# Performance work log

Hardware: AMD Instinct MI355X
Metric: run time of the kernel (lower is better)

## Reference

```python
import jax, jax.numpy as jnp
import numpy as np

B, IN, H = 16384, 1024, 1024


def setup_inputs() -> dict:
    key = jax.random.key(0)
    ks = jax.random.split(key, 16)
    stdv = 1.0 / np.sqrt(H)
    u = lambda k, shape: jax.random.uniform(k, shape, jnp.float32, -stdv, stdv)
    return {
        "input": jax.random.normal(ks[0], (B, IN), jnp.float32),
        "prev_h": jax.random.normal(ks[1], (B, H), jnp.float32),
        "prev_c": jax.random.normal(ks[2], (B, H), jnp.float32),
        "weight_xi": u(ks[3], (IN, H)), "weight_hi": u(ks[4], (H, H)),
        "weight_xf": u(ks[5], (IN, H)), "weight_hf": u(ks[6], (H, H)),
        "weight_xu": u(ks[7], (IN, H)), "weight_hu": u(ks[8], (H, H)),
        "weight_xo": u(ks[9], (IN, H)), "weight_ho": u(ks[10], (H, H)),
        "bias_i": u(ks[11], (H,)), "bias_f": u(ks[12], (H,)),
        "bias_o": u(ks[13], (H,)), "bias_u": u(ks[14], (H,)),
    }


def reference(input, prev_h, prev_c,
              weight_xi, weight_hi, weight_xf, weight_hf,
              weight_xu, weight_hu, weight_xo, weight_ho,
              bias_i, bias_f, bias_o, bias_u):
    i = jax.nn.sigmoid(input @ weight_xi + prev_h @ weight_hi + bias_i)
    f = jax.nn.sigmoid(input @ weight_xf + prev_h @ weight_hf + bias_f)
    o = jax.nn.sigmoid(input @ weight_xo + prev_h @ weight_ho + bias_o)
    u = jnp.tanh(input @ weight_xu + prev_h @ weight_hu + bias_u)
    c = f * prev_c + i * u
    h = o * jnp.tanh(c)
    return (h, c)
```

## Files before the change

kernel.cpp:

```cpp
#include <hip/hip_runtime.h>
#include <hip/hip_bf16.h>
#include <stdint.h>
#include <type_traits>


typedef short bf16x8 __attribute__((ext_vector_type(8)));
typedef unsigned short u16x8 __attribute__((ext_vector_type(8)));
typedef float f32x16 __attribute__((ext_vector_type(16)));

__device__ __forceinline__ unsigned short f2bf(float f) {
    union { float f; uint32_t u; } v; v.f = f;
    uint32_t r = v.u + 0x7FFFu + ((v.u >> 16) & 1u);
    return (unsigned short)(r >> 16);
}

__device__ __forceinline__ float fsig(float x) { return 1.0f / (1.0f + __expf(-x)); }
__device__ __forceinline__ float ftanh(float x) { return 2.0f * fsig(2.0f * x) - 1.0f; }

__global__ __launch_bounds__(256) void pack_a_kernel(const float* __restrict__ input,
                                                     const float* __restrict__ prev_h,
                                                     unsigned short* __restrict__ Apk2) {
    int u = blockIdx.x * 256 + threadIdx.x;
    int l = u & 63, q = (u >> 6) & 1, rg = (u >> 7) & 7, t = (u >> 10) & 63, rt = u >> 16;
    int row = rt * 256 + rg * 32 + (l & 31);
    int k0 = t * 32 + (q * 2 + (l >> 5)) * 8;
    const float* src = (k0 < 1024) ? (input + (size_t)row * 1024 + k0)
                                   : (prev_h + (size_t)row * 1024 + (k0 - 1024));
    float4 lo = *(const float4*)src;
    float4 hi = *(const float4*)(src + 4);
    u16x8 o;
    o[0] = f2bf(lo.x); o[1] = f2bf(lo.y); o[2] = f2bf(lo.z); o[3] = f2bf(lo.w);
    o[4] = f2bf(hi.x); o[5] = f2bf(hi.y); o[6] = f2bf(hi.z); o[7] = f2bf(hi.w);
    *(u16x8*)(Apk2 + (size_t)u * 8) = o;
}

__global__ __launch_bounds__(256) void pack_b_kernel(
        const float* __restrict__ wxi, const float* __restrict__ wxf,
        const float* __restrict__ wxo, const float* __restrict__ wxu,
        const float* __restrict__ whi, const float* __restrict__ whf,
        const float* __restrict__ who, const float* __restrict__ whu,
        unsigned short* __restrict__ Bpk2) {
    int u = blockIdx.x * 256 + threadIdx.x;
    int l = u & 63, q = (u >> 6) & 1, ch = (u >> 7) & 1, g = (u >> 8) & 3,
        t = (u >> 10) & 63, ct = u >> 16;
    const float* wx = (g == 0) ? wxi : (g == 1) ? wxf : (g == 2) ? wxo : wxu;
    const float* wh = (g == 0) ? whi : (g == 1) ? whf : (g == 2) ? who : whu;
    int j = ct * 64 + ch * 32 + (l & 31);
    int k0 = t * 32 + (q * 2 + (l >> 5)) * 8;
    const float* src = (k0 < 1024) ? (wx + (size_t)k0 * 1024 + j)
                                   : (wh + (size_t)(k0 - 1024) * 1024 + j);
    u16x8 o;
#pragma unroll
    for (int e = 0; e < 8; ++e) o[e] = f2bf(src[(size_t)e * 1024]);
    *(u16x8*)(Bpk2 + (size_t)u * 8) = o;
}


#define GLL(gp, lp) __builtin_amdgcn_global_load_lds( \
        (__attribute__((address_space(1))) void*)(gp), \
        (__attribute__((address_space(3))) void*)(lp), 16, 0, 0)

#define BAR() do { asm volatile("" ::: "memory"); __builtin_amdgcn_s_barrier(); \
                   asm volatile("" ::: "memory"); } while (0)

__global__ __launch_bounds__(512, 2) void lstm_gemm_kernel(
        const unsigned short* __restrict__ Apk2,
        const unsigned short* __restrict__ Bpk2,
        const float* __restrict__ prev_c,
        const float* __restrict__ bi, const float* __restrict__ bf_,
        const float* __restrict__ bo, const float* __restrict__ bu,
        float* __restrict__ out_h, float* __restrict__ out_c) {
    __shared__ __align__(16) unsigned char smem[131072];
    const int tid = threadIdx.x;
    const int w = tid >> 6, l = tid & 63;
    const int l31 = l & 31, l5 = l >> 5;
    const int wr = w >> 1, wc = w & 1;

    const int bid = blockIdx.x;
    const int sw = ((bid & 7) << 7) + (bid >> 3);
    const int tileRow = sw & 63, tileCol = sw >> 6;
    const int rowBase = tileRow * 256;
    const int jBase = tileCol * 64;

    int aoff[2][2], boff[4][2];
#pragma unroll
    for (int m = 0; m < 2; ++m)
#pragma unroll
        for (int ks = 0; ks < 2; ++ks)
            aoff[m][ks] = (wr * 2 + m) * 2048 + (ks * 2 + l5) * 512 + l31 * 16;
#pragma unroll
    for (int g = 0; g < 4; ++g)
#pragma unroll
        for (int ks = 0; ks < 2; ++ks)
            boff[g][ks] = 16384 + g * 4096 + wc * 2048 + (ks * 2 + l5) * 512 + l31 * 16;

    const unsigned short* aSrc = Apk2 + (size_t)tileRow * 64 * 8192 + w * 1024 + l * 8;
    const unsigned short* bSrc = Bpk2 + (size_t)tileCol * 64 * 8192
                               + (w >> 1) * 2048 + (w & 1) * 1024 + l * 8;
    const int aD = w * 2048;
    const int bD = 16384 + (w >> 1) * 4096 + (w & 1) * 2048;

#define STAGE4(T) do { const int _bb = ((T) & 3) * 32768; \
        const size_t _o = (size_t)(T) * 8192; \
        GLL(aSrc + _o,       smem + _bb + aD); \
        GLL(aSrc + _o + 512, smem + _bb + aD + 1024); \
        GLL(bSrc + _o,       smem + _bb + bD); \
        GLL(bSrc + _o + 512, smem + _bb + bD + 1024); } while (0)

    f32x16 acc[2][4];
#pragma unroll
    for (int m = 0; m < 2; ++m)
#pragma unroll
        for (int g = 0; g < 4; ++g)
#pragma unroll
            for (int q = 0; q < 16; ++q) acc[m][g][q] = 0.f;

    STAGE4(0); STAGE4(1);
    asm volatile("s_waitcnt vmcnt(4)" ::: "memory");
    BAR();

    auto slice = [&](int t, auto vnc, auto stgc) {
        constexpr int VN = decltype(vnc)::value;
        constexpr bool STG = decltype(stgc)::value;
        const int bt = (t & 3) * 32768;
        if constexpr (STG) STAGE4(t + 2);
        bf16x8 av[2][2], bv[4][2];
#pragma unroll
        for (int m = 0; m < 2; ++m)
#pragma unroll
            for (int ks = 0; ks < 2; ++ks)
                av[m][ks] = *(const bf16x8*)(smem + bt + aoff[m][ks]);
#pragma unroll
        for (int g = 0; g < 4; ++g)
#pragma unroll
            for (int ks = 0; ks < 2; ++ks)
                bv[g][ks] = *(const bf16x8*)(smem + bt + boff[g][ks]);
#pragma unroll
        for (int ks = 0; ks < 2; ++ks)
#pragma unroll
            for (int m = 0; m < 2; ++m)
#pragma unroll
                for (int g = 0; g < 4; ++g)
                    acc[m][g] = __builtin_amdgcn_mfma_f32_32x32x16_bf16(
                        av[m][ks], bv[g][ks], acc[m][g], 0, 0, 0);
        if constexpr (VN == 4)      asm volatile("s_waitcnt vmcnt(4)" ::: "memory");
        else if constexpr (VN == 0) asm volatile("s_waitcnt vmcnt(0)" ::: "memory");
        if constexpr (VN >= 0) BAR();
    };

    using c4 = std::integral_constant<int, 4>;
    using c0 = std::integral_constant<int, 0>;
    using cm = std::integral_constant<int, -1>;
    using bT = std::integral_constant<bool, true>;
    using bF = std::integral_constant<bool, false>;

#pragma unroll 1
    for (int t = 0; t < 62; ++t) slice(t, c4{}, bT{});
    slice(62, c0{}, bF{});
    slice(63, cm{}, bF{});

    const int colIdx = jBase + wc * 32 + l31;
    const float vbi = bi[colIdx], vbf = bf_[colIdx], vbo = bo[colIdx], vbu = bu[colIdx];
    const int rowB = rowBase + wr * 64 + 4 * l5;
#pragma unroll
    for (int m = 0; m < 2; ++m) {
#pragma unroll
        for (int q = 0; q < 16; ++q) {
            const int row = rowB + m * 32 + (q & 3) + 8 * (q >> 2);
            const size_t idx = (size_t)row * 1024 + colIdx;
            float zi = acc[m][0][q] + vbi;
            float zf = acc[m][1][q] + vbf;
            float zo = acc[m][2][q] + vbo;
            float zu = acc[m][3][q] + vbu;
            float iv = fsig(zi), fv = fsig(zf), ov = fsig(zo), uv = ftanh(zu);
            float cv = fv * prev_c[idx] + iv * uv;
            out_c[idx] = cv;
            out_h[idx] = ov * ftanh(cv);
        }
    }
#undef STAGE4
}

extern "C" void kernel_launch(void* const* d_in, const int* in_sizes, int n_in,
                              void* d_out, int out_size, void* d_ws, size_t ws_size,
                              hipStream_t stream) {
    const float* input  = (const float*)d_in[0];
    const float* prev_h = (const float*)d_in[1];
    const float* prev_c = (const float*)d_in[2];
    const float* wxi = (const float*)d_in[3];
    const float* whi = (const float*)d_in[4];
    const float* wxf = (const float*)d_in[5];
    const float* whf = (const float*)d_in[6];
    const float* wxu = (const float*)d_in[7];
    const float* whu = (const float*)d_in[8];
    const float* wxo = (const float*)d_in[9];
    const float* who = (const float*)d_in[10];
    const float* bi  = (const float*)d_in[11];
    const float* bf_ = (const float*)d_in[12];
    const float* bo  = (const float*)d_in[13];
    const float* bu  = (const float*)d_in[14];

    unsigned short* Apk2 = (unsigned short*)d_ws;
    unsigned short* Bpk2 = (unsigned short*)((char*)d_ws + (size_t)67108864);

    float* out_h = (float*)d_out;
    float* out_c = out_h + (size_t)16384 * 1024;

    pack_a_kernel<<<dim3(16384), dim3(256), 0, stream>>>(input, prev_h, Apk2);
    pack_b_kernel<<<dim3(4096), dim3(256), 0, stream>>>(wxi, wxf, wxo, wxu,
                                                        whi, whf, who, whu, Bpk2);
    lstm_gemm_kernel<<<dim3(1024), dim3(512), 0, stream>>>(Apk2, Bpk2, prev_c,
                                                           bi, bf_, bo, bu, out_h, out_c);
}
```

Before: 349.9 us.

## Deepen LDS prefetch to three stages and double-buffer MFMA fragments in registers

Global-to-LDS staging now runs three K-slices ahead instead of two, using the existing four LDS buffers. The shared-memory reads of operand fragments for slice t+1 are issued during the MFMAs of slice t, into alternating register sets. sched_group_barrier hints interleave those LDS reads with the MFMA instructions. The aim is to hide LDS and global latency behind the matrix math, at the cost of more VGPRs for the doubled fragment buffers, which could lower occupancy or cause spills.

```diff
diff --git a/kernel.cpp b/kernel.cpp
--- a/kernel.cpp
+++ b/kernel.cpp
@@ -115,26 +115,35 @@
 #pragma unroll
             for (int q = 0; q < 16; ++q) acc[m][g][q] = 0.f;
 
-    STAGE4(0); STAGE4(1);
+    bf16x8 aE[4], bE[8], aO[4], bO[8];
+
+    auto ldfr = [&](int t, bf16x8 (&da)[4], bf16x8 (&db)[8]) {
+        const int bt = (t & 3) * 32768;
+#pragma unroll
+        for (int m = 0; m < 2; ++m)
+#pragma unroll
+            for (int ks = 0; ks < 2; ++ks)
+                da[m * 2 + ks] = *(const bf16x8*)(smem + bt + aoff[m][ks]);
+#pragma unroll
+        for (int g = 0; g < 4; ++g)
+#pragma unroll
+            for (int ks = 0; ks < 2; ++ks)
+                db[g * 2 + ks] = *(const bf16x8*)(smem + bt + boff[g][ks]);
+    };
+
+    STAGE4(0); STAGE4(1); STAGE4(2);
     asm volatile("s_waitcnt vmcnt(4)" ::: "memory");
     BAR();
-
-    auto slice = [&](int t, auto vnc, auto stgc) {
+    ldfr(0, aE, bE);
+
+    auto slice = [&](int t, auto vnc, auto stgc, auto nxtc,
+                     bf16x8 (&ca)[4], bf16x8 (&cb)[8],
+                     bf16x8 (&na)[4], bf16x8 (&nb)[8]) {
         constexpr int VN = decltype(vnc)::value;
         constexpr bool STG = decltype(stgc)::value;
-        const int bt = (t & 3) * 32768;
-        if constexpr (STG) STAGE4(t + 2);
-        bf16x8 av[2][2], bv[4][2];
-#pragma unroll
-        for (int m = 0; m < 2; ++m)
-#pragma unroll
-            for (int ks = 0; ks < 2; ++ks)
-                av[m][ks] = *(const bf16x8*)(smem + bt + aoff[m][ks]);
-#pragma unroll
-        for (int g = 0; g < 4; ++g)
-#pragma unroll
-            for (int ks = 0; ks < 2; ++ks)
-                bv[g][ks] = *(const bf16x8*)(smem + bt + boff[g][ks]);
+        constexpr bool NXT = decltype(nxtc)::value;
+        if constexpr (STG) STAGE4(t + 3);
+        if constexpr (NXT) ldfr(t + 1, na, nb);
 #pragma unroll
         for (int ks = 0; ks < 2; ++ks)
 #pragma unroll
@@ -142,7 +151,11 @@
 #pragma unroll
                 for (int g = 0; g < 4; ++g)
                     acc[m][g] = __builtin_amdgcn_mfma_f32_32x32x16_bf16(
-                        av[m][ks], bv[g][ks], acc[m][g], 0, 0, 0);
+                        ca[m * 2 + ks], cb[g * 2 + ks], acc[m][g], 0, 0, 0);
+        if constexpr (NXT) {
+            __builtin_amdgcn_sched_group_barrier(0x100, 12, 0);
+            __builtin_amdgcn_sched_group_barrier(0x8,   16, 0);
+        }
         if constexpr (VN == 4)      asm volatile("s_waitcnt vmcnt(4)" ::: "memory");
         else if constexpr (VN == 0) asm volatile("s_waitcnt vmcnt(0)" ::: "memory");
         if constexpr (VN >= 0) BAR();
@@ -155,9 +168,14 @@
     using bF = std::integral_constant<bool, false>;
 
 #pragma unroll 1
-    for (int t = 0; t < 62; ++t) slice(t, c4{}, bT{});
-    slice(62, c0{}, bF{});
-    slice(63, cm{}, bF{});
+    for (int t = 0; t < 60; t += 2) {
+        slice(t,     c4{}, bT{}, bT{}, aE, bE, aO, bO);
+        slice(t + 1, c4{}, bT{}, bT{}, aO, bO, aE, bE);
+    }
+    slice(60, c4{}, bT{}, bT{}, aE, bE, aO, bO);
+    slice(61, c0{}, bF{}, bT{}, aO, bO, aE, bE);
+    slice(62, cm{}, bF{}, bT{}, aE, bE, aO, bO);
+    slice(63, cm{}, bF{}, bF{}, aO, bO, aE, bE);
 
     const int colIdx = jBase + wc * 32 + l31;
     const float vbi = bi[colIdx], vbf = bf_[colIdx], vbo = bo[colIdx], vbu = bu[colIdx];
```

New measurement: 372.9 us. +6.6%, slower.

## Load A fragments directly into registers, stage only B through LDS

Applied to the files above, without the earlier changes.

The A operand is now read straight from global memory into double-buffered registers (one slice ahead) instead of being staged through LDS. LDS then holds only the B tiles, which halves its footprint to 64 KB, and the wait counts are adjusted for the mixed load stream. The aim is to cut LDS traffic and capacity pressure, which could allow more resident blocks. In exchange it raises register pressure, and because each wave pair loads its A rows separately, some A data is fetched from global memory twice.

```diff
diff --git a/kernel.cpp b/kernel.cpp
--- a/kernel.cpp
+++ b/kernel.cpp
@@ -70,7 +70,7 @@
         const float* __restrict__ bi, const float* __restrict__ bf_,
         const float* __restrict__ bo, const float* __restrict__ bu,
         float* __restrict__ out_h, float* __restrict__ out_c) {
-    __shared__ __align__(16) unsigned char smem[131072];
+    __shared__ __align__(16) unsigned char smem[65536];
     const int tid = threadIdx.x;
     const int w = tid >> 6, l = tid & 63;
     const int l31 = l & 31, l5 = l >> 5;
@@ -82,28 +82,20 @@
     const int rowBase = tileRow * 256;
     const int jBase = tileCol * 64;
 
-    int aoff[2][2], boff[4][2];
-#pragma unroll
-    for (int m = 0; m < 2; ++m)
+    int boff[4][2];
+#pragma unroll
+    for (int g = 0; g < 4; ++g)
 #pragma unroll
         for (int ks = 0; ks < 2; ++ks)
-            aoff[m][ks] = (wr * 2 + m) * 2048 + (ks * 2 + l5) * 512 + l31 * 16;
-#pragma unroll
-    for (int g = 0; g < 4; ++g)
-#pragma unroll
-        for (int ks = 0; ks < 2; ++ks)
-            boff[g][ks] = 16384 + g * 4096 + wc * 2048 + (ks * 2 + l5) * 512 + l31 * 16;
-
-    const unsigned short* aSrc = Apk2 + (size_t)tileRow * 64 * 8192 + w * 1024 + l * 8;
-    const unsigned short* bSrc = Bpk2 + (size_t)tileCol * 64 * 8192
-                               + (w >> 1) * 2048 + (w & 1) * 1024 + l * 8;
-    const int aD = w * 2048;
-    const int bD = 16384 + (w >> 1) * 4096 + (w & 1) * 2048;
-
-#define STAGE4(T) do { const int _bb = ((T) & 3) * 32768; \
+            boff[g][ks] = g * 4096 + wc * 2048 + (ks * 2 + l5) * 512 + l31 * 16;
+
+    const unsigned short* aSrcF = Apk2 + (size_t)tileRow * 524288 + (wr * 2) * 1024 + l * 8;
+
+    const unsigned short* bSrc = Bpk2 + (size_t)tileCol * 524288 + w * 1024 + l * 8;
+    const int bD = w * 2048;
+
+#define STAGE_B(T) do { const int _bb = ((T) & 3) * 16384; \
         const size_t _o = (size_t)(T) * 8192; \
-        GLL(aSrc + _o,       smem + _bb + aD); \
-        GLL(aSrc + _o + 512, smem + _bb + aD + 1024); \
         GLL(bSrc + _o,       smem + _bb + bD); \
         GLL(bSrc + _o + 512, smem + _bb + bD + 1024); } while (0)
 
@@ -115,21 +107,31 @@
 #pragma unroll
             for (int q = 0; q < 16; ++q) acc[m][g][q] = 0.f;
 
-    STAGE4(0); STAGE4(1);
-    asm volatile("s_waitcnt vmcnt(4)" ::: "memory");
+    bf16x8 aE[4], aO[4];
+
+    auto ldA = [&](int t, bf16x8 (&da)[4]) {
+        const unsigned short* ap = aSrcF + (size_t)t * 8192;
+#pragma unroll
+        for (int m = 0; m < 2; ++m)
+#pragma unroll
+            for (int ks = 0; ks < 2; ++ks)
+                da[m * 2 + ks] = *(const bf16x8*)(ap + m * 1024 + ks * 512);
+    };
+
+    ldA(0, aE);
+    STAGE_B(0); STAGE_B(1);
+    asm volatile("s_waitcnt vmcnt(2)" ::: "memory");
     BAR();
 
-    auto slice = [&](int t, auto vnc, auto stgc) {
+    auto slice = [&](int t, auto vnc, auto stgc, auto ldac,
+                     bf16x8 (&aCur)[4], bf16x8 (&aNxt)[4]) {
         constexpr int VN = decltype(vnc)::value;
         constexpr bool STG = decltype(stgc)::value;
-        const int bt = (t & 3) * 32768;
-        if constexpr (STG) STAGE4(t + 2);
-        bf16x8 av[2][2], bv[4][2];
-#pragma unroll
-        for (int m = 0; m < 2; ++m)
-#pragma unroll
-            for (int ks = 0; ks < 2; ++ks)
-                av[m][ks] = *(const bf16x8*)(smem + bt + aoff[m][ks]);
+        constexpr bool LDA = decltype(ldac)::value;
+        const int bt = (t & 3) * 16384;
+        if constexpr (LDA) ldA(t + 1, aNxt);
+        if constexpr (STG) STAGE_B(t + 2);
+        bf16x8 bv[4][2];
 #pragma unroll
         for (int g = 0; g < 4; ++g)
 #pragma unroll
@@ -142,22 +144,25 @@
 #pragma unroll
                 for (int g = 0; g < 4; ++g)
                     acc[m][g] = __builtin_amdgcn_mfma_f32_32x32x16_bf16(
-                        av[m][ks], bv[g][ks], acc[m][g], 0, 0, 0);
-        if constexpr (VN == 4)      asm volatile("s_waitcnt vmcnt(4)" ::: "memory");
-        else if constexpr (VN == 0) asm volatile("s_waitcnt vmcnt(0)" ::: "memory");
+                        aCur[m * 2 + ks], bv[g][ks], acc[m][g], 0, 0, 0);
+        if constexpr (VN == 6)      asm volatile("s_waitcnt vmcnt(6)" ::: "memory");
+        else if constexpr (VN == 4) asm volatile("s_waitcnt vmcnt(4)" ::: "memory");
         if constexpr (VN >= 0) BAR();
     };
 
+    using c6 = std::integral_constant<int, 6>;
     using c4 = std::integral_constant<int, 4>;
-    using c0 = std::integral_constant<int, 0>;
     using cm = std::integral_constant<int, -1>;
     using bT = std::integral_constant<bool, true>;
     using bF = std::integral_constant<bool, false>;
 
 #pragma unroll 1
-    for (int t = 0; t < 62; ++t) slice(t, c4{}, bT{});
-    slice(62, c0{}, bF{});
-    slice(63, cm{}, bF{});
+    for (int t = 0; t < 62; t += 2) {
+        slice(t,     c6{}, bT{}, bT{}, aE, aO);
+        slice(t + 1, c6{}, bT{}, bT{}, aO, aE);
+    }
+    slice(62, c4{}, bF{}, bT{}, aE, aO);
+    slice(63, cm{}, bF{}, bF{}, aO, aE);
 
     const int colIdx = jBase + wc * 32 + l31;
     const float vbi = bi[colIdx], vbf = bf_[colIdx], vbo = bo[colIdx], vbu = bu[colIdx];
@@ -178,7 +183,7 @@
             out_h[idx] = ov * ftanh(cv);
         }
     }
-#undef STAGE4
+#undef STAGE_B
 }
 
 extern "C" void kernel_launch(void* const* d_in, const int* in_sizes, int n_in,
```

After: 372.1 us. 6.4% more time.

## Switch GEMM main loop to double-buffered 64-wide K tiles with interleaved staging

Applied to the files above, without the earlier changes.

Restructures the fused LSTM GEMM main loop from a 4-deep ring of 32-wide K slices (one barrier per slice) to a 2-buffer scheme with 64-wide K tiles of 64KB each. Global-to-LDS loads for the next tile are spread between the four MFMA sub-steps of the current tile, so there is one barrier per 64 K instead of per 32. The intent is to halve barrier and wait overhead and interleave loads with compute. The cost is a shallower prefetch distance with a full vmcnt(0) wait each tile, which may expose memory latency. The LDS offset math changes to match a new packed layout, and correctness depends on that layout agreeing with the unseen pack kernels.

```diff
diff --git a/kernel.cpp b/kernel.cpp
--- a/kernel.cpp
+++ b/kernel.cpp
@@ -82,30 +82,29 @@
     const int rowBase = tileRow * 256;
     const int jBase = tileCol * 64;
 
-    int aoff[2][2], boff[4][2];
+    int aoff[2][4], boff[4][4];
 #pragma unroll
     for (int m = 0; m < 2; ++m)
 #pragma unroll
-        for (int ks = 0; ks < 2; ++ks)
-            aoff[m][ks] = (wr * 2 + m) * 2048 + (ks * 2 + l5) * 512 + l31 * 16;
+        for (int ks = 0; ks < 4; ++ks)
+            aoff[m][ks] = (ks >> 1) * 16384 + ((wr * 2 + m) * 2 + (ks & 1)) * 1024 + l * 16;
 #pragma unroll
     for (int g = 0; g < 4; ++g)
 #pragma unroll
-        for (int ks = 0; ks < 2; ++ks)
-            boff[g][ks] = 16384 + g * 4096 + wc * 2048 + (ks * 2 + l5) * 512 + l31 * 16;
-
-    const unsigned short* aSrc = Apk2 + (size_t)tileRow * 64 * 8192 + w * 1024 + l * 8;
-    const unsigned short* bSrc = Bpk2 + (size_t)tileCol * 64 * 8192
-                               + (w >> 1) * 2048 + (w & 1) * 1024 + l * 8;
-    const int aD = w * 2048;
-    const int bD = 16384 + (w >> 1) * 4096 + (w & 1) * 2048;
-
-#define STAGE4(T) do { const int _bb = ((T) & 3) * 32768; \
-        const size_t _o = (size_t)(T) * 8192; \
-        GLL(aSrc + _o,       smem + _bb + aD); \
-        GLL(aSrc + _o + 512, smem + _bb + aD + 1024); \
-        GLL(bSrc + _o,       smem + _bb + bD); \
-        GLL(bSrc + _o + 512, smem + _bb + bD + 1024); } while (0)
+        for (int ks = 0; ks < 4; ++ks)
+            boff[g][ks] = 32768 + (ks >> 1) * 16384 + (g * 4 + wc * 2 + (ks & 1)) * 1024 + l * 16;
+
+    const unsigned short* aSrcW = Apk2 + (size_t)tileRow * 524288
+                                + (size_t)(w >> 2) * 8192 + ((w & 3) * 4) * 512 + l * 8;
+    const unsigned short* bSrcW = Bpk2 + (size_t)tileCol * 524288
+                                + (size_t)(w >> 2) * 8192 + ((w & 3) * 4) * 512 + l * 8;
+    const int aDstW = w * 4096;
+    const int bDstW = 32768 + w * 4096;
+
+#define STAGE_A1(KT, J) GLL(aSrcW + (size_t)(KT) * 16384 + (J) * 512, \
+                            smem + ((((KT) & 1)) * 65536) + aDstW + (J) * 1024)
+#define STAGE_B1(KT, J) GLL(bSrcW + (size_t)(KT) * 16384 + (J) * 512, \
+                            smem + ((((KT) & 1)) * 65536) + bDstW + (J) * 1024)
 
     f32x16 acc[2][4];
 #pragma unroll
@@ -115,49 +114,67 @@
 #pragma unroll
             for (int q = 0; q < 16; ++q) acc[m][g][q] = 0.f;
 
-    STAGE4(0); STAGE4(1);
-    asm volatile("s_waitcnt vmcnt(4)" ::: "memory");
+    STAGE_A1(0, 0); STAGE_A1(0, 1); STAGE_A1(0, 2); STAGE_A1(0, 3);
+    STAGE_B1(0, 0); STAGE_B1(0, 1); STAGE_B1(0, 2); STAGE_B1(0, 3);
+    asm volatile("s_waitcnt vmcnt(0)" ::: "memory");
     BAR();
 
-    auto slice = [&](int t, auto vnc, auto stgc) {
-        constexpr int VN = decltype(vnc)::value;
-        constexpr bool STG = decltype(stgc)::value;
-        const int bt = (t & 3) * 32768;
-        if constexpr (STG) STAGE4(t + 2);
-        bf16x8 av[2][2], bv[4][2];
-#pragma unroll
-        for (int m = 0; m < 2; ++m)
-#pragma unroll
-            for (int ks = 0; ks < 2; ++ks)
-                av[m][ks] = *(const bf16x8*)(smem + bt + aoff[m][ks]);
-#pragma unroll
-        for (int g = 0; g < 4; ++g)
-#pragma unroll
-            for (int ks = 0; ks < 2; ++ks)
-                bv[g][ks] = *(const bf16x8*)(smem + bt + boff[g][ks]);
-#pragma unroll
-        for (int ks = 0; ks < 2; ++ks)
-#pragma unroll
-            for (int m = 0; m < 2; ++m)
-#pragma unroll
-                for (int g = 0; g < 4; ++g)
-                    acc[m][g] = __builtin_amdgcn_mfma_f32_32x32x16_bf16(
-                        av[m][ks], bv[g][ks], acc[m][g], 0, 0, 0);
-        if constexpr (VN == 4)      asm volatile("s_waitcnt vmcnt(4)" ::: "memory");
-        else if constexpr (VN == 0) asm volatile("s_waitcnt vmcnt(0)" ::: "memory");
-        if constexpr (VN >= 0) BAR();
+    auto ktile = [&](int kt, auto modeC) {
+        constexpr int MODE = decltype(modeC)::value;
+        const int bufb = (kt & 1) * 65536;
+        bf16x8 av[2], bv[4];
+#pragma unroll
+        for (int m = 0; m < 2; ++m) av[m] = *(const bf16x8*)(smem + bufb + aoff[m][0]);
+#pragma unroll
+        for (int g = 0; g < 4; ++g) bv[g] = *(const bf16x8*)(smem + bufb + boff[g][0]);
+        if constexpr (MODE == 0) { STAGE_A1(kt + 1, 0); STAGE_A1(kt + 1, 1); }
+#pragma unroll
+        for (int m = 0; m < 2; ++m)
+#pragma unroll
+            for (int g = 0; g < 4; ++g)
+                acc[m][g] = __builtin_amdgcn_mfma_f32_32x32x16_bf16(av[m], bv[g], acc[m][g], 0, 0, 0);
+#pragma unroll
+        for (int m = 0; m < 2; ++m) av[m] = *(const bf16x8*)(smem + bufb + aoff[m][1]);
+#pragma unroll
+        for (int g = 0; g < 4; ++g) bv[g] = *(const bf16x8*)(smem + bufb + boff[g][1]);
+        if constexpr (MODE == 0) { STAGE_A1(kt + 1, 2); STAGE_A1(kt + 1, 3);
+                                   STAGE_B1(kt + 1, 0); STAGE_B1(kt + 1, 1); }
+#pragma unroll
+        for (int m = 0; m < 2; ++m)
+#pragma unroll
+            for (int g = 0; g < 4; ++g)
+                acc[m][g] = __builtin_amdgcn_mfma_f32_32x32x16_bf16(av[m], bv[g], acc[m][g], 0, 0, 0);
+#pragma unroll
+        for (int m = 0; m < 2; ++m) av[m] = *(const bf16x8*)(smem + bufb + aoff[m][2]);
+#pragma unroll
+        for (int g = 0; g < 4; ++g) bv[g] = *(const bf16x8*)(smem + bufb + boff[g][2]);
+        if constexpr (MODE == 0) { STAGE_B1(kt + 1, 2); STAGE_B1(kt + 1, 3); }
+#pragma unroll
+        for (int m = 0; m < 2; ++m)
+#pragma unroll
+            for (int g = 0; g < 4; ++g)
+                acc[m][g] = __builtin_amdgcn_mfma_f32_32x32x16_bf16(av[m], bv[g], acc[m][g], 0, 0, 0);
+#pragma unroll
+        for (int m = 0; m < 2; ++m) av[m] = *(const bf16x8*)(smem + bufb + aoff[m][3]);
+#pragma unroll
+        for (int g = 0; g < 4; ++g) bv[g] = *(const bf16x8*)(smem + bufb + boff[g][3]);
+        if constexpr (MODE == 0) {
+            asm volatile("s_waitcnt vmcnt(0)" ::: "memory");
+            BAR();
+        }
+#pragma unroll
+        for (int m = 0; m < 2; ++m)
+#pragma unroll
+            for (int g = 0; g < 4; ++g)
+                acc[m][g] = __builtin_amdgcn_mfma_f32_32x32x16_bf16(av[m], bv[g], acc[m][g], 0, 0, 0);
     };
 
-    using c4 = std::integral_constant<int, 4>;
-    using c0 = std::integral_constant<int, 0>;
-    using cm = std::integral_constant<int, -1>;
-    using bT = std::integral_constant<bool, true>;
-    using bF = std::integral_constant<bool, false>;
+    using m0 = std::integral_constant<int, 0>;
+    using m1 = std::integral_constant<int, 1>;
 
 #pragma unroll 1
-    for (int t = 0; t < 62; ++t) slice(t, c4{}, bT{});
-    slice(62, c0{}, bF{});
-    slice(63, cm{}, bF{});
+    for (int kt = 0; kt < 31; ++kt) ktile(kt, m0{});
+    ktile(31, m1{});
 
     const int colIdx = jBase + wc * 32 + l31;
     const float vbi = bi[colIdx], vbf = bf_[colIdx], vbo = bo[colIdx], vbu = bu[colIdx];
@@ -178,7 +195,8 @@
             out_h[idx] = ov * ftanh(cv);
         }
     }
-#undef STAGE4
+#undef STAGE_A1
+#undef STAGE_B1
 }
 
 extern "C" void kernel_launch(void* const* d_in, const int* in_sizes, int n_in,
```

Result: no change. 353.6 us (+1.1%).
